# Performance work log

Measured on AMD Instinct MI355X. Metric: run time of the kernel, lower is better.

Reference implementation:

```python
import jax, jax.numpy as jnp
import numpy as np

N_EMBD = 1024
N_HEAD = 16
B, T = 4, 2048

def setup_inputs() -> dict:
    key = jax.random.key(0)
    ks = jax.random.split(key, 5)
    s_attn = 1.0 / np.sqrt(N_EMBD)
    s_proj = 1.0 / np.sqrt(N_EMBD)
    return {
        "x": jax.random.normal(ks[0], (B, T, N_EMBD), dtype=jnp.float32),
        "w_attn": jax.random.uniform(ks[1], (N_EMBD, 3 * N_EMBD), jnp.float32, -s_attn, s_attn),
        "b_attn": jax.random.uniform(ks[2], (3 * N_EMBD,), jnp.float32, -s_attn, s_attn),
        "w_proj": jax.random.uniform(ks[3], (N_EMBD, N_EMBD), jnp.float32, -s_proj, s_proj),
        "b_proj": jax.random.uniform(ks[4], (N_EMBD,), jnp.float32, -s_proj, s_proj),
    }

def reference(x, w_attn, b_attn, w_proj, b_proj):
    Bx, Tx, C = x.shape
    hd = C // N_HEAD  # head dim
    qkv = x @ w_attn + b_attn                       # [B,T,3C]
    q, k, v = jnp.split(qkv, 3, axis=-1)
    # [B,T,C] -> [B,H,T,hd]
    def heads(t):
        return t.reshape(Bx, Tx, N_HEAD, hd).transpose(0, 2, 1, 3)
    q, k, v = heads(q), heads(k), heads(v)
    att = jnp.einsum('bhqd,bhkd->bhqk', q, k) * (1.0 / np.sqrt(hd))
    causal = jnp.tril(jnp.ones((Tx, Tx), dtype=bool))
    att = jnp.where(causal, att, -jnp.inf)
    att = jax.nn.softmax(att, axis=-1)
    y = jnp.einsum('bhqk,bhkd->bhqd', att, v)       # [B,H,T,hd]
    y = y.transpose(0, 2, 1, 3).reshape(Bx, Tx, C)
    return y @ w_proj + b_proj
```

## Files before the change

kernel.cpp:

```cpp
#include <hip/hip_runtime.h>
#include <cstdint>

typedef unsigned short u16;
typedef short s16x8 __attribute__((ext_vector_type(8)));
typedef short s16x4 __attribute__((ext_vector_type(4)));
typedef float f32x4 __attribute__((ext_vector_type(4)));

#define B_   4
#define T_   2048
#define C_   1024
#define H_   16
#define HD_  64
#define M_   8192
#define N3_  3072

#define QSCALE 0.18033688011112042f

__device__ inline u16 f2b(float f) {
  union { float f; uint32_t u; } v; v.f = f;
  uint32_t u = v.u;
  return (u16)((u + 0x7FFFu + ((u >> 16) & 1u)) >> 16);
}

__device__ inline f32x4 mfma16(s16x4 a, s16x4 b, f32x4 c) {
#if __has_builtin(__builtin_amdgcn_mfma_f32_16x16x16bf16_1k)
  return __builtin_amdgcn_mfma_f32_16x16x16bf16_1k(a, b, c, 0, 0, 0);
#else
  f32x4 d;
  asm("v_mfma_f32_16x16x16_bf16 %0, %1, %2, %3"
      : "=v"(d) : "v"(a), "v"(b), "v"(c));
  return d;
#endif
}

__device__ inline void gload_lds16(const void* g, void* l) {
  __builtin_amdgcn_global_load_lds(
      (const __attribute__((address_space(1))) void*)g,
      (__attribute__((address_space(3))) void*)l, 16, 0, 0);
}

__global__ __launch_bounds__(256) void cvt_f32_bf16(
    const float* __restrict__ in, u16* __restrict__ out, int n) {
  int i = (blockIdx.x * 256 + threadIdx.x) * 8;
  if (i >= n) return;
  float4 a = *(const float4*)(in + i);
  float4 b = *(const float4*)(in + i + 4);
  s16x8 r;
  r[0] = (short)f2b(a.x); r[1] = (short)f2b(a.y);
  r[2] = (short)f2b(a.z); r[3] = (short)f2b(a.w);
  r[4] = (short)f2b(b.x); r[5] = (short)f2b(b.y);
  r[6] = (short)f2b(b.z); r[7] = (short)f2b(b.w);
  *(s16x8*)(out + i) = r;
}

__global__ __launch_bounds__(256) void cvt_transpose(
    const float* __restrict__ W, u16* __restrict__ WT, int K, int N) {
  __shared__ u16 tile[64][65];
  int n0 = blockIdx.x * 64, k0 = blockIdx.y * 64;
  int j = threadIdx.x & 63, i0 = threadIdx.x >> 6;
#pragma unroll
  for (int i = i0; i < 64; i += 4)
    tile[i][j] = f2b(W[(size_t)(k0 + i) * N + n0 + j]);
  __syncthreads();
#pragma unroll
  for (int i = i0; i < 64; i += 4)
    WT[(size_t)(n0 + i) * K + k0 + j] = tile[j][i];
}

template <int MODE>
__global__ __launch_bounds__(256, 2) void gemm_bt(
    const u16* __restrict__ A, const u16* __restrict__ Bt,
    const float* __restrict__ bias, float* __restrict__ outf,
    u16* __restrict__ qo, u16* __restrict__ ko, u16* __restrict__ vo,
    int M, int N, int K) {
  __shared__ u16 As[128 * 32];
  __shared__ u16 Bs[128 * 32];
  int nwg = gridDim.x;
  int bid0 = blockIdx.x;
  int bid = (bid0 & 7) * (nwg >> 3) + (bid0 >> 3);
  int nbn = N >> 7;
  int bm = bid / nbn, bn = bid % nbn;
  int m0 = bm * 128, n0 = bn * 128;
  int tid = threadIdx.x;
  int lane = tid & 63, w = tid >> 6;
  int wm = (w >> 1) * 64, wn = (w & 1) * 64;
  int l15 = lane & 15, g = lane >> 4;

  f32x4 acc[4][4] = {};

  for (int kb = 0; kb < K; kb += 32) {
    __syncthreads();
#pragma unroll
    for (int it = 0; it < 2; ++it) {
      int idx = it * 256 + tid;
      int row = idx >> 2, kc = (idx & 3) * 8;
      gload_lds16(A  + (size_t)(m0 + row) * K + kb + kc, &As[idx * 8]);
      gload_lds16(Bt + (size_t)(n0 + row) * K + kb + kc, &Bs[idx * 8]);
    }
    __syncthreads();

    s16x8 af[4], bf[4];
#pragma unroll
    for (int mi = 0; mi < 4; ++mi)
      af[mi] = *(const s16x8*)&As[(wm + mi * 16 + l15) * 32 + g * 8];
#pragma unroll
    for (int ni = 0; ni < 4; ++ni)
      bf[ni] = *(const s16x8*)&Bs[(wn + ni * 16 + l15) * 32 + g * 8];
#pragma unroll
    for (int mi = 0; mi < 4; ++mi)
#pragma unroll
      for (int ni = 0; ni < 4; ++ni)
        acc[mi][ni] = __builtin_amdgcn_mfma_f32_16x16x32_bf16(
            af[mi], bf[ni], acc[mi][ni], 0, 0, 0);
  }

#pragma unroll
  for (int mi = 0; mi < 4; ++mi)
#pragma unroll
    for (int ni = 0; ni < 4; ++ni) {
      int col = n0 + wn + ni * 16 + l15;
      float bv = bias[col];
      int row0 = m0 + wm + mi * 16 + g * 4;
      if (MODE == 0) {
#pragma unroll
        for (int r = 0; r < 4; ++r)
          outf[(size_t)(row0 + r) * N + col] = acc[mi][ni][r] + bv;
      } else {
        int which = col >> 10, hc = col & 1023;
        int h = hc >> 6, d = hc & 63;
        int b = row0 >> 11, t0 = row0 & 2047;
        if (which == 2) {
          s16x4 pv;
#pragma unroll
          for (int r = 0; r < 4; ++r) pv[r] = (short)f2b(acc[mi][ni][r] + bv);
          *(s16x4*)(vo + ((size_t)((b * 16 + h) * 64 + d)) * 2048 + t0) = pv;
        } else {
          u16* dst = (which == 0) ? qo : ko;
          float sc2 = (which == 0) ? QSCALE : 1.0f;
#pragma unroll
          for (int r = 0; r < 4; ++r)
            dst[(((size_t)(b * 16 + h)) * 2048 + (t0 + r)) * 64 + d] =
                f2b((acc[mi][ni][r] + bv) * sc2);
        }
      }
    }
}

__global__ __launch_bounds__(256, 4) void attn_fwd(
    const u16* __restrict__ Q, const u16* __restrict__ Kg,
    const u16* __restrict__ Vt, u16* __restrict__ Y) {
  __shared__ u16 Ks[64 * 64];
  __shared__ u16 Vs[64 * 64];

  int bid = blockIdx.x;
  int bh = bid & 63;
  int qt = 31 - (bid >> 6);
  int tid = threadIdx.x, lane = tid & 63, w = tid >> 6;
  int l15 = lane & 15, g = lane >> 4;

  const u16* Qh = Q  + (size_t)bh * T_ * HD_;
  const u16* Kh = Kg + (size_t)bh * T_ * HD_;
  const u16* Vh = Vt + (size_t)bh * HD_ * T_;

  int q0 = qt * 64 + w * 16;
  int qrow = q0 + l15;

  s16x8 qa[2];
#pragma unroll
  for (int ks = 0; ks < 2; ++ks)
    qa[ks] = *(const s16x8*)(Qh + (size_t)qrow * HD_ + g * 8 + ks * 32);

  f32x4 oacc[4] = {};
  float m = -3.0e30f, l = 0.f;

  int sr = tid >> 3, sc = tid & 7;
  int wswz = (sr & 7) << 4;
  int rswz = (l15 & 7) << 4;
  char* KsB = (char*)Ks;
  char* VsB = (char*)Vs;

  s16x8 kr0 = *(const s16x8*)(Kh + (size_t)sr * HD_ + sc * 8);
  s16x8 kr1 = *(const s16x8*)(Kh + (size_t)(sr + 32) * HD_ + sc * 8);
  s16x8 vr0 = *(const s16x8*)(Vh + (size_t)sr * T_ + sc * 8);
  s16x8 vr1 = *(const s16x8*)(Vh + (size_t)(sr + 32) * T_ + sc * 8);

  int ntile = qt + 1;
  for (int kt = 0; kt < ntile; ++kt) {
    int kvb = kt * 64;
    __syncthreads();
    *(s16x8*)(KsB + sr * 128 + ((sc * 16) ^ wswz))        = kr0;
    *(s16x8*)(KsB + (sr + 32) * 128 + ((sc * 16) ^ wswz)) = kr1;
    *(s16x8*)(VsB + sr * 128 + ((sc * 16) ^ wswz))        = vr0;
    *(s16x8*)(VsB + (sr + 32) * 128 + ((sc * 16) ^ wswz)) = vr1;
    __syncthreads();

    {
      int kvn = (kt + 1 < ntile) ? (kt + 1) * 64 : 0;
      kr0 = *(const s16x8*)(Kh + (size_t)(kvn + sr) * HD_ + sc * 8);
      kr1 = *(const s16x8*)(Kh + (size_t)(kvn + sr + 32) * HD_ + sc * 8);
      vr0 = *(const s16x8*)(Vh + (size_t)sr * T_ + kvn + sc * 8);
      vr1 = *(const s16x8*)(Vh + (size_t)(sr + 32) * T_ + kvn + sc * 8);
    }

    f32x4 sacc[4] = {};
#pragma unroll
    for (int cf = 0; cf < 4; ++cf)
#pragma unroll
      for (int ks = 0; ks < 2; ++ks) {
        s16x8 kb = *(const s16x8*)(KsB + (cf * 16 + l15) * 128 +
                                   ((g * 16 + ks * 64) ^ rswz));
        sacc[cf] = __builtin_amdgcn_mfma_f32_16x16x32_bf16(kb, qa[ks], sacc[cf], 0, 0, 0);
      }

    if (kt == qt) {
#pragma unroll
      for (int cf = 0; cf < 4; ++cf)
#pragma unroll
        for (int r = 0; r < 4; ++r) {
          int kv = kvb + cf * 16 + g * 4 + r;
          if (kv > qrow) sacc[cf][r] = -1e30f;
        }
    }

    float t0 = fmaxf(fmaxf(sacc[0][0], sacc[0][1]), fmaxf(sacc[0][2], sacc[0][3]));
    float t1 = fmaxf(fmaxf(sacc[1][0], sacc[1][1]), fmaxf(sacc[1][2], sacc[1][3]));
    float t2 = fmaxf(fmaxf(sacc[2][0], sacc[2][1]), fmaxf(sacc[2][2], sacc[2][3]));
    float t3 = fmaxf(fmaxf(sacc[3][0], sacc[3][1]), fmaxf(sacc[3][2], sacc[3][3]));
    float mx = fmaxf(fmaxf(t0, t1), fmaxf(t2, t3));
    mx = fmaxf(mx, __shfl_xor(mx, 16, 64));
    mx = fmaxf(mx, __shfl_xor(mx, 32, 64));

    if (!__all(mx <= m + 8.0f)) {
      float mn = fmaxf(m, mx);
      float alpha = __builtin_amdgcn_exp2f(m - mn);
      m = mn;
      l *= alpha;
#pragma unroll
      for (int df = 0; df < 4; ++df)
#pragma unroll
        for (int r = 0; r < 4; ++r) oacc[df][r] *= alpha;
    }

    float rs = 0.f;
#pragma unroll
    for (int cf = 0; cf < 4; ++cf)
#pragma unroll
      for (int r = 0; r < 4; ++r) {
        float p = __builtin_amdgcn_exp2f(sacc[cf][r] - m);
        sacc[cf][r] = p;
        rs += p;
      }
    rs += __shfl_xor(rs, 16, 64);
    rs += __shfl_xor(rs, 32, 64);
    l += rs;

#pragma unroll
    for (int cf = 0; cf < 4; ++cf) {
      s16x4 pb;
#pragma unroll
      for (int r = 0; r < 4; ++r) pb[r] = (short)f2b(sacc[cf][r]);
#pragma unroll
      for (int df = 0; df < 4; ++df) {
        s16x4 va = *(const s16x4*)(VsB + (df * 16 + l15) * 128 +
                                   ((cf * 32 + g * 8) ^ rswz));
        oacc[df] = mfma16(va, pb, oacc[df]);
      }
    }
  }

  int b = bh >> 4, h = bh & 15;
  float inv = 1.0f / l;
  u16* yrow = Y + ((size_t)b * T_ + qrow) * C_ + h * 64;
#pragma unroll
  for (int df = 0; df < 4; ++df) {
    s16x4 o;
#pragma unroll
    for (int r = 0; r < 4; ++r) o[r] = (short)f2b(oacc[df][r] * inv);
    *(s16x4*)(yrow + df * 16 + g * 4) = o;
  }
}

extern "C" void kernel_launch(void* const* d_in, const int* in_sizes, int n_in,
                              void* d_out, int out_size, void* d_ws, size_t ws_size,
                              hipStream_t stream) {
  const float* x      = (const float*)d_in[0];
  const float* w_attn = (const float*)d_in[1];
  const float* b_attn = (const float*)d_in[2];
  const float* w_proj = (const float*)d_in[3];
  const float* b_proj = (const float*)d_in[4];
  float* out = (float*)d_out;

  u16* ws  = (u16*)d_ws;
  u16* xb  = ws;
  u16* wat = xb  + (size_t)M_ * C_;
  u16* wpt = wat + (size_t)N3_ * C_;
  u16* q   = wpt + (size_t)C_ * C_;
  u16* k   = q   + (size_t)M_ * C_;
  u16* v   = k   + (size_t)M_ * C_;
  u16* ya  = xb;

  cvt_f32_bf16<<<dim3((M_ * C_) / (256 * 8)), dim3(256), 0, stream>>>(x, xb, M_ * C_);
  cvt_transpose<<<dim3(N3_ / 64, C_ / 64), dim3(256), 0, stream>>>(w_attn, wat, C_, N3_);
  cvt_transpose<<<dim3(C_ / 64, C_ / 64), dim3(256), 0, stream>>>(w_proj, wpt, C_, C_);

  gemm_bt<1><<<dim3((M_ / 128) * (N3_ / 128)), dim3(256), 0, stream>>>(
      xb, wat, b_attn, nullptr, q, k, v, M_, N3_, C_);

  attn_fwd<<<dim3(64 * 32), dim3(256), 0, stream>>>(q, k, v, ya);

  gemm_bt<0><<<dim3((M_ / 128) * (C_ / 128)), dim3(256), 0, stream>>>(
      ya, wpt, b_proj, out, nullptr, nullptr, nullptr, M_, C_, C_);
}
```

Before: 187.0 us.

## Double-buffer GEMM with 128x256 tiles, 512 threads, and swizzled LDS

Replaces the single-buffered 128x128 GEMM with a 512-thread kernel computing 128x256 tiles. Global-to-LDS loads for the next K tile are issued into a second buffer while MFMAs run on the current one, with split K halves and s_setprio around the compute. An XOR swizzle on the LDS chunk index is meant to avoid bank conflicts. The goal is to hide global load latency and raise data reuse per block, at the cost of more LDS use (64 KB) and reduced occupancy, plus the risk of subtle synchronisation bugs.

Result: slower. 191.7 us (+2.5%).

```diff
diff --git a/kernel.cpp b/kernel.cpp
--- a/kernel.cpp
+++ b/kernel.cpp
@@ -68,52 +68,84 @@
 }
 
 template <int MODE>
-__global__ __launch_bounds__(256, 2) void gemm_bt(
+__global__ __launch_bounds__(512, 2) void gemm_pipe(
     const u16* __restrict__ A, const u16* __restrict__ Bt,
     const float* __restrict__ bias, float* __restrict__ outf,
     u16* __restrict__ qo, u16* __restrict__ ko, u16* __restrict__ vo,
     int M, int N, int K) {
-  __shared__ u16 As[128 * 32];
-  __shared__ u16 Bs[128 * 32];
+  __shared__ u16 As[2][2][128 * 32];
+  __shared__ u16 Bs[2][2][256 * 32];
+
   int nwg = gridDim.x;
   int bid0 = blockIdx.x;
   int bid = (bid0 & 7) * (nwg >> 3) + (bid0 >> 3);
-  int nbn = N >> 7;
+  int nbn = N >> 8;
   int bm = bid / nbn, bn = bid % nbn;
-  int m0 = bm * 128, n0 = bn * 128;
+  int m0 = bm * 128, n0 = bn * 256;
   int tid = threadIdx.x;
   int lane = tid & 63, w = tid >> 6;
-  int wm = (w >> 1) * 64, wn = (w & 1) * 64;
+  int wm = (w >> 2) * 64, wn = (w & 3) * 64;
   int l15 = lane & 15, g = lane >> 4;
+  int nt = K >> 6;
+
+  int srow = lane >> 2;
+  int schunk = (lane & 3) ^ ((lane >> 3) & 3);
+  const u16* Ab  = A  + (size_t)(m0 + w * 16 + srow) * K + schunk * 8;
+  const u16* Bb0 = Bt + (size_t)(n0 + w * 32 + srow) * K + schunk * 8;
+  const u16* Bb1 = Bt + (size_t)(n0 + w * 32 + 16 + srow) * K + schunk * 8;
+
+#define STAGE_A(bb, kh, kt) \
+  gload_lds16(Ab + (kt) * 64 + (kh) * 32, &As[bb][kh][w * 512])
+#define STAGE_B(bb, kh, kt) do { \
+  gload_lds16(Bb0 + (kt) * 64 + (kh) * 32, &Bs[bb][kh][w * 1024]); \
+  gload_lds16(Bb1 + (kt) * 64 + (kh) * 32, &Bs[bb][kh][w * 1024 + 512]); \
+} while (0)
+
+  int csw = (g ^ ((l15 >> 1) & 3)) * 8;
+  int ra[4], rb[4];
+#pragma unroll
+  for (int i = 0; i < 4; ++i) {
+    ra[i] = (wm + i * 16 + l15) * 32 + csw;
+    rb[i] = (wn + i * 16 + l15) * 32 + csw;
+  }
 
   f32x4 acc[4][4] = {};
 
-  for (int kb = 0; kb < K; kb += 32) {
-    __syncthreads();
-#pragma unroll
-    for (int it = 0; it < 2; ++it) {
-      int idx = it * 256 + tid;
-      int row = idx >> 2, kc = (idx & 3) * 8;
-      gload_lds16(A  + (size_t)(m0 + row) * K + kb + kc, &As[idx * 8]);
-      gload_lds16(Bt + (size_t)(n0 + row) * K + kb + kc, &Bs[idx * 8]);
-    }
-    __syncthreads();
-
-    s16x8 af[4], bf[4];
-#pragma unroll
-    for (int mi = 0; mi < 4; ++mi)
-      af[mi] = *(const s16x8*)&As[(wm + mi * 16 + l15) * 32 + g * 8];
-#pragma unroll
-    for (int ni = 0; ni < 4; ++ni)
-      bf[ni] = *(const s16x8*)&Bs[(wn + ni * 16 + l15) * 32 + g * 8];
-#pragma unroll
-    for (int mi = 0; mi < 4; ++mi)
-#pragma unroll
-      for (int ni = 0; ni < 4; ++ni)
-        acc[mi][ni] = __builtin_amdgcn_mfma_f32_16x16x32_bf16(
-            af[mi], bf[ni], acc[mi][ni], 0, 0, 0);
+#define PHASE(curb, kh, ktn) do { \
+  s16x8 af[4], bf[4]; \
+  _Pragma("unroll") for (int i = 0; i < 4; ++i) \
+    af[i] = *(const s16x8*)&As[curb][kh][ra[i]]; \
+  _Pragma("unroll") for (int i = 0; i < 4; ++i) \
+    bf[i] = *(const s16x8*)&Bs[curb][kh][rb[i]]; \
+  STAGE_A((curb) ^ 1, kh, ktn); \
+  STAGE_B((curb) ^ 1, kh, ktn); \
+  asm volatile("s_waitcnt vmcnt(3)" ::: "memory"); \
+  __builtin_amdgcn_s_barrier(); \
+  __builtin_amdgcn_s_setprio(1); \
+  _Pragma("unroll") for (int mi = 0; mi < 4; ++mi) \
+  _Pragma("unroll") for (int ni = 0; ni < 4; ++ni) \
+    acc[mi][ni] = __builtin_amdgcn_mfma_f32_16x16x32_bf16( \
+        af[mi], bf[ni], acc[mi][ni], 0, 0, 0); \
+  __builtin_amdgcn_s_setprio(0); \
+  __builtin_amdgcn_s_barrier(); \
+} while (0)
+
+  STAGE_A(0, 0, 0); STAGE_B(0, 0, 0);
+  STAGE_A(0, 1, 0); STAGE_B(0, 1, 0);
+  asm volatile("s_waitcnt vmcnt(3)" ::: "memory");
+  __builtin_amdgcn_s_barrier();
+
+  for (int t = 0; t < nt; ++t) {
+    int cur = t & 1;
+    int ktn = (t + 1 < nt) ? t + 1 : 0;
+    PHASE(cur, 0, ktn);
+    PHASE(cur, 1, ktn);
   }
-
+#undef PHASE
+#undef STAGE_A
+#undef STAGE_B
+
+  int which = (MODE == 1) ? (n0 >> 10) : 0;
 #pragma unroll
   for (int mi = 0; mi < 4; ++mi)
 #pragma unroll
@@ -126,7 +158,7 @@
         for (int r = 0; r < 4; ++r)
           outf[(size_t)(row0 + r) * N + col] = acc[mi][ni][r] + bv;
       } else {
-        int which = col >> 10, hc = col & 1023;
+        int hc = col & 1023;
         int h = hc >> 6, d = hc & 63;
         int b = row0 >> 11, t0 = row0 & 2047;
         if (which == 2) {
@@ -303,11 +335,11 @@
   cvt_transpose<<<dim3(N3_ / 64, C_ / 64), dim3(256), 0, stream>>>(w_attn, wat, C_, N3_);
   cvt_transpose<<<dim3(C_ / 64, C_ / 64), dim3(256), 0, stream>>>(w_proj, wpt, C_, C_);
 
-  gemm_bt<1><<<dim3((M_ / 128) * (N3_ / 128)), dim3(256), 0, stream>>>(
+  gemm_pipe<1><<<dim3((M_ / 128) * (N3_ / 256)), dim3(512), 0, stream>>>(
       xb, wat, b_attn, nullptr, q, k, v, M_, N3_, C_);
 
   attn_fwd<<<dim3(64 * 32), dim3(256), 0, stream>>>(q, k, v, ya);
 
-  gemm_bt<0><<<dim3((M_ / 128) * (C_ / 128)), dim3(256), 0, stream>>>(
+  gemm_pipe<0><<<dim3((M_ / 128) * (C_ / 256)), dim3(512), 0, stream>>>(
       ya, wpt, b_proj, out, nullptr, nullptr, nullptr, M_, C_, C_);
 }
```

## Replace GEMMs with 8-wave double-buffered, swizzled-LDS pipelined GEMM kernel

Applied to the files above, without the earlier changes.

Both projection GEMMs move from a 256-thread, 128x128-tile, single-buffered kernel to a 512-thread kernel with 256x256 or 128x256 tiles and K-step 64. LDS is double-buffered and XOR-swizzled. The loop interleaves LDS fragment loads, MFMA quadrants under raised priority, and the next-tile global-to-LDS prefetch, using explicit vmcnt waits and barriers. The aim is to hide global load latency, cut LDS bank conflicts and raise reuse per tile. In exchange it uses more LDS and registers per workgroup, has fewer workgroups in flight, and depends on hand-tuned barrier and waitcnt placement being correct.

After: 194.4 us. 1.04x slower.

```diff
diff --git a/kernel.cpp b/kernel.cpp
--- a/kernel.cpp
+++ b/kernel.cpp
@@ -67,72 +67,123 @@
     WT[(size_t)(n0 + i) * K + k0 + j] = tile[j][i];
 }
 
-template <int MODE>
-__global__ __launch_bounds__(256, 2) void gemm_bt(
+template <int MODE, int BM>
+__global__ __launch_bounds__(512, 1) void gemm8p(
     const u16* __restrict__ A, const u16* __restrict__ Bt,
     const float* __restrict__ bias, float* __restrict__ outf,
     u16* __restrict__ qo, u16* __restrict__ ko, u16* __restrict__ vo,
     int M, int N, int K) {
-  __shared__ u16 As[128 * 32];
-  __shared__ u16 Bs[128 * 32];
+  constexpr int WR  = BM / 2;
+  constexpr int MH  = WR / 32;
+  constexpr int MF  = WR / 16;
+  constexpr int ALH = BM / 128;
+  constexpr int VM  = 2 * ALH + 4;
+
+  __shared__ u16 As[2][BM * 64];
+  __shared__ u16 Bs[2][256 * 64];
+
   int nwg = gridDim.x;
   int bid0 = blockIdx.x;
   int bid = (bid0 & 7) * (nwg >> 3) + (bid0 >> 3);
-  int nbn = N >> 7;
+  int nbn = N >> 8;
   int bm = bid / nbn, bn = bid % nbn;
-  int m0 = bm * 128, n0 = bn * 128;
-  int tid = threadIdx.x;
-  int lane = tid & 63, w = tid >> 6;
-  int wm = (w >> 1) * 64, wn = (w & 1) * 64;
+  int m0 = bm * BM, n0 = bn * 256;
+  int tid = threadIdx.x, lane = tid & 63, w = tid >> 6;
   int l15 = lane & 15, g = lane >> 4;
-
-  f32x4 acc[4][4] = {};
-
-  for (int kb = 0; kb < K; kb += 32) {
-    __syncthreads();
-#pragma unroll
-    for (int it = 0; it < 2; ++it) {
-      int idx = it * 256 + tid;
-      int row = idx >> 2, kc = (idx & 3) * 8;
-      gload_lds16(A  + (size_t)(m0 + row) * K + kb + kc, &As[idx * 8]);
-      gload_lds16(Bt + (size_t)(n0 + row) * K + kb + kc, &Bs[idx * 8]);
-    }
-    __syncthreads();
-
-    s16x8 af[4], bf[4];
-#pragma unroll
-    for (int mi = 0; mi < 4; ++mi)
-      af[mi] = *(const s16x8*)&As[(wm + mi * 16 + l15) * 32 + g * 8];
-#pragma unroll
-    for (int ni = 0; ni < 4; ++ni)
-      bf[ni] = *(const s16x8*)&Bs[(wn + ni * 16 + l15) * 32 + g * 8];
-#pragma unroll
-    for (int mi = 0; mi < 4; ++mi)
-#pragma unroll
-      for (int ni = 0; ni < 4; ++ni)
-        acc[mi][ni] = __builtin_amdgcn_mfma_f32_16x16x32_bf16(
-            af[mi], bf[ni], acc[mi][ni], 0, 0, 0);
+  int wm = (w >> 2) * WR, wn = (w & 3) * 64;
+  int nt = K >> 6;
+
+  int lr = lane >> 3;
+  int csrc = ((lane & 7) ^ (lr & 7)) * 8;
+  const u16* Ab = A  + (size_t)(m0 + w * ALH * 8 + lr) * K + csrc;
+  const u16* Bb = Bt + (size_t)(n0 + w * 16 + lr) * K + csrc;
+
+  int x8 = l15 & 7;
+  int ck0 = (g ^ x8) * 8;
+  int ck1 = ((4 + g) ^ x8) * 8;
+
+  f32x4 acc[MF][4] = {};
+  s16x8 af[MH][2], bf[2][2][2];
+
+#define BAR() asm volatile("s_barrier" ::: "memory")
+#define LDA(mh_) do { \
+  _Pragma("unroll") for (int mi = 0; mi < MH; ++mi) { \
+    int rw = (wm + (mh_) * MH * 16 + mi * 16 + l15) * 64; \
+    af[mi][0] = *(const s16x8*)&As[c][rw + ck0]; \
+    af[mi][1] = *(const s16x8*)&As[c][rw + ck1]; \
+  } } while (0)
+#define LDB(np_) do { \
+  _Pragma("unroll") for (int ni = 0; ni < 2; ++ni) { \
+    int rw = (wn + (np_) * 32 + ni * 16 + l15) * 64; \
+    bf[np_][ni][0] = *(const s16x8*)&Bs[c][rw + ck0]; \
+    bf[np_][ni][1] = *(const s16x8*)&Bs[c][rw + ck1]; \
+  } } while (0)
+#define QUAD(mh_, np_) do { \
+  __builtin_amdgcn_s_setprio(1); \
+  _Pragma("unroll") for (int mi = 0; mi < MH; ++mi) \
+  _Pragma("unroll") for (int ni = 0; ni < 2; ++ni) \
+  _Pragma("unroll") for (int ks = 0; ks < 2; ++ks) \
+    acc[(mh_) * MH + mi][(np_) * 2 + ni] = \
+        __builtin_amdgcn_mfma_f32_16x16x32_bf16( \
+            af[mi][ks], bf[np_][ni][ks], \
+            acc[(mh_) * MH + mi][(np_) * 2 + ni], 0, 0, 0); \
+  __builtin_amdgcn_s_setprio(0); \
+} while (0)
+#define STAGE(bb, tt) do { \
+  int ko_ = (tt) * 64; \
+  _Pragma("unroll") for (int h = 0; h < 2; ++h) \
+  _Pragma("unroll") for (int i = 0; i < ALH; ++i) \
+    gload_lds16(Ab + (size_t)(h * WR + i * 8) * K + ko_, \
+                (u16*)&As[bb][h * WR * 64 + (w * ALH + i) * 512 + lane * 8]); \
+  _Pragma("unroll") for (int h = 0; h < 2; ++h) \
+  _Pragma("unroll") for (int i = 0; i < 2; ++i) \
+    gload_lds16(Bb + (size_t)(h * 128 + i * 8) * K + ko_, \
+                (u16*)&Bs[bb][h * 8192 + (w * 2 + i) * 512 + lane * 8]); \
+} while (0)
+
+  STAGE(0, 0);
+  STAGE(1, 1);
+  asm volatile("s_waitcnt vmcnt(%0)" :: "i"(VM) : "memory");
+  BAR();
+
+  for (int t = 0; t < nt; ++t) {
+    int c = t & 1;
+    LDA(0); LDB(0);
+    BAR(); QUAD(0, 0); BAR();
+    LDB(1);
+    BAR(); QUAD(0, 1); BAR();
+    LDA(1);
+    BAR(); QUAD(1, 0); BAR();
+    { int tt = t + 2; if (tt >= nt) tt -= nt; STAGE(c, tt); }
+    asm volatile("s_waitcnt vmcnt(%0)" :: "i"(VM) : "memory");
+    BAR(); QUAD(1, 1); BAR();
   }
-
-#pragma unroll
-  for (int mi = 0; mi < 4; ++mi)
-#pragma unroll
-    for (int ni = 0; ni < 4; ++ni) {
-      int col = n0 + wn + ni * 16 + l15;
+#undef BAR
+#undef LDA
+#undef LDB
+#undef QUAD
+#undef STAGE
+
+  int which = (MODE == 1) ? (n0 >> 10) : 0;
+#pragma unroll
+  for (int mf = 0; mf < MF; ++mf)
+#pragma unroll
+    for (int na = 0; na < 4; ++na) {
+      int col = n0 + wn + na * 16 + l15;
       float bv = bias[col];
-      int row0 = m0 + wm + mi * 16 + g * 4;
+      int row0 = m0 + wm + mf * 16 + g * 4;
       if (MODE == 0) {
 #pragma unroll
         for (int r = 0; r < 4; ++r)
-          outf[(size_t)(row0 + r) * N + col] = acc[mi][ni][r] + bv;
+          outf[(size_t)(row0 + r) * N + col] = acc[mf][na][r] + bv;
       } else {
-        int which = col >> 10, hc = col & 1023;
+        int hc = col & 1023;
         int h = hc >> 6, d = hc & 63;
         int b = row0 >> 11, t0 = row0 & 2047;
         if (which == 2) {
           s16x4 pv;
 #pragma unroll
-          for (int r = 0; r < 4; ++r) pv[r] = (short)f2b(acc[mi][ni][r] + bv);
+          for (int r = 0; r < 4; ++r) pv[r] = (short)f2b(acc[mf][na][r] + bv);
           *(s16x4*)(vo + ((size_t)((b * 16 + h) * 64 + d)) * 2048 + t0) = pv;
         } else {
           u16* dst = (which == 0) ? qo : ko;
@@ -140,7 +191,7 @@
 #pragma unroll
           for (int r = 0; r < 4; ++r)
             dst[(((size_t)(b * 16 + h)) * 2048 + (t0 + r)) * 64 + d] =
-                f2b((acc[mi][ni][r] + bv) * sc2);
+                f2b((acc[mf][na][r] + bv) * sc2);
         }
       }
     }
@@ -303,11 +354,11 @@
   cvt_transpose<<<dim3(N3_ / 64, C_ / 64), dim3(256), 0, stream>>>(w_attn, wat, C_, N3_);
   cvt_transpose<<<dim3(C_ / 64, C_ / 64), dim3(256), 0, stream>>>(w_proj, wpt, C_, C_);
 
-  gemm_bt<1><<<dim3((M_ / 128) * (N3_ / 128)), dim3(256), 0, stream>>>(
+  gemm8p<1, 256><<<dim3((M_ / 256) * (N3_ / 256)), dim3(512), 0, stream>>>(
       xb, wat, b_attn, nullptr, q, k, v, M_, N3_, C_);
 
   attn_fwd<<<dim3(64 * 32), dim3(256), 0, stream>>>(q, k, v, ya);
 
-  gemm_bt<0><<<dim3((M_ / 128) * (C_ / 128)), dim3(256), 0, stream>>>(
+  gemm8p<0, 128><<<dim3((M_ / 128) * (C_ / 256)), dim3(512), 0, stream>>>(
       ya, wpt, b_proj, out, nullptr, nullptr, nullptr, M_, C_, C_);
 }
```
